# Performance work log

Measured on AMD Instinct MI355X. Metric: run time of the kernel, lower is better.

Reference implementation:

```python
import jax, jax.numpy as jnp
import numpy as np

B, L, N, C, H = 32, 11, 577, 768, 12
HD = C // H  # head dim 64
THRESH = 0.5
NEG = -1e9


def layer_norm(x, g, b, eps=1e-6):
    m = jnp.mean(x, axis=-1, keepdims=True)
    v = jnp.var(x, axis=-1, keepdims=True)
    return (x - m) * jax.lax.rsqrt(v + eps) * g + b


def setup_inputs() -> dict:
    key = jax.random.key(0)
    ks = jax.random.split(key, 8)
    s = 0.02
    return {
        "last_x": jax.random.normal(ks[0], (B, N, C), jnp.float32),
        "attn_scores": jax.random.normal(ks[1], (B, L, N), jnp.float32),
        "norm1_g": jnp.ones((C,), jnp.float32),
        "norm1_b": jnp.zeros((C,), jnp.float32),
        "qkv_w": jax.random.normal(ks[2], (3 * C, C), jnp.float32) * s,
        "qkv_b": jnp.zeros((3 * C,), jnp.float32),
        "proj_w": jax.random.normal(ks[3], (C, C), jnp.float32) * s,
        "proj_b": jnp.zeros((C,), jnp.float32),
        "norm2_g": jnp.ones((C,), jnp.float32),
        "norm2_b": jnp.zeros((C,), jnp.float32),
        "fc1_w": jax.random.normal(ks[4], (4 * C, C), jnp.float32) * s,
        "fc1_b": jnp.zeros((4 * C,), jnp.float32),
        "fc2_w": jax.random.normal(ks[5], (C, 4 * C), jnp.float32) * s,
        "fc2_b": jnp.zeros((C,), jnp.float32),
        "bbn_g": jnp.ones((C,), jnp.float32),
        "bbn_b": jnp.zeros((C,), jnp.float32),
        "out_g": jnp.ones((C,), jnp.float32),
        "out_b": jnp.zeros((C,), jnp.float32),
    }


def prune(attn_scores):
    # scores per block, drop CLS column, softmax over patches, mean over blocks
    ps = jax.nn.softmax(attn_scores[:, :, 1:], axis=-1).mean(axis=1)  # [B, P]
    order = jnp.argsort(ps, axis=1)  # ascending
    sorted_s = jnp.take_along_axis(ps, order, axis=1)
    keep_sorted = jnp.cumsum(sorted_s, axis=1) > THRESH  # drop low-mass prefix
    # scatter back to original patch positions
    pm = jnp.zeros_like(keep_sorted)
    pm = pm.at[jnp.arange(ps.shape[0])[:, None], order].set(keep_sorted)
    # CLS token always kept
    return jnp.concatenate([jnp.ones((ps.shape[0], 1), bool), pm], axis=1)  # [B, N]


def masked_block(x, token_masks, norm1_g, norm1_b, qkv_w, qkv_b, proj_w, proj_b,
                 norm2_g, norm2_b, fc1_w, fc1_b, fc2_w, fc2_b):
    b, n, c = x.shape
    h = layer_norm(x, norm1_g, norm1_b)
    qkv = (h @ qkv_w.T + qkv_b).reshape(b, n, 3, H, HD).transpose(2, 0, 3, 1, 4)
    q, k, v = qkv[0], qkv[1], qkv[2]  # [B, H, N, HD]
    att = jnp.einsum("bhqd,bhkd->bhqk", q, k) * (HD ** -0.5)
    mf = token_masks.astype(x.dtype)
    pair = (mf[:, None, :, None] * mf[:, None, None, :]) > 0  # [B,1,N,N]
    att = jnp.where(pair, att, NEG)
    p = jax.nn.softmax(att, axis=-1)
    p = jnp.where(pair, p, 0.0)  # zero fully-masked rows
    y = jnp.einsum("bhqk,bhkd->bhqd", p, v).transpose(0, 2, 1, 3).reshape(b, n, c)
    y = y @ proj_w.T + proj_b
    x = x + y
    m = layer_norm(x, norm2_g, norm2_b)
    m = jax.nn.gelu(m @ fc1_w.T + fc1_b, approximate=False) @ fc2_w.T + fc2_b
    return x + m


def reference(last_x, attn_scores, norm1_g, norm1_b, qkv_w, qkv_b, proj_w, proj_b,
              norm2_g, norm2_b, fc1_w, fc1_b, fc2_w, fc2_b, bbn_g, bbn_b, out_g, out_b):
    token_masks = prune(attn_scores)  # [B, N] bool
    x = masked_block(last_x, token_masks, norm1_g, norm1_b, qkv_w, qkv_b,
                     proj_w, proj_b, norm2_g, norm2_b, fc1_w, fc1_b, fc2_w, fc2_b)
    x = layer_norm(x, bbn_g, bbn_b)  # backbone final norm
    mf = token_masks.astype(x.dtype)
    pooled = (x * mf[:, :, None]).sum(axis=1) / mf.sum(axis=1, keepdims=True)
    return layer_norm(pooled, out_g, out_b)  # [B, C]
```

## Files before the change

### kernel.cpp

```cpp
#include <hip/hip_runtime.h>

#define B_   32
#define L_   11
#define N_   577
#define C_   768
#define H_   12
#define HD_  64
#define M_   (B_ * N_)
#define NP_  608
#define QT_  32
#define NQT_ 19
#define MCH_ 4616

typedef unsigned int uint32;

typedef short bf16x8 __attribute__((ext_vector_type(8)));
typedef float f32x4  __attribute__((ext_vector_type(4)));

__device__ __forceinline__ unsigned short f2bf(float f) {
    union { float f; uint32 u; } c; c.f = f;
    uint32 u = c.u;
    uint32 r = (u + 0x7FFFu + ((u >> 16) & 1u)) >> 16;
    return (unsigned short)r;
}
__device__ __forceinline__ float bf2f(unsigned short u) {
    union { uint32 u; float f; } c; c.u = ((uint32)u) << 16;
    return c.f;
}
__device__ __forceinline__ float ldval(const float* p, size_t i) { return p[i]; }
__device__ __forceinline__ float ldval(const unsigned short* p, size_t i) { return bf2f(p[i]); }

__device__ __forceinline__ bf16x8 ld_frag(const unsigned short* p) {
    union { uint4 u; bf16x8 v; } c;
    c.u = *reinterpret_cast<const uint4*>(p);
    return c.v;
}

__device__ __forceinline__ void gload_lds16(const unsigned short* g, unsigned short* l) {
    __builtin_amdgcn_global_load_lds(
        (const __attribute__((address_space(1))) unsigned int*)g,
        (__attribute__((address_space(3))) unsigned int*)l, 16, 0, 0);
}

__global__ __launch_bounds__(256) void cast4_kernel(const float* __restrict__ qkvw,
                                                    const float* __restrict__ projw,
                                                    const float* __restrict__ fc1w,
                                                    const float* __restrict__ fc2w,
                                                    unsigned short* __restrict__ dq,
                                                    unsigned short* __restrict__ dp,
                                                    unsigned short* __restrict__ d1,
                                                    unsigned short* __restrict__ d2) {
    int i = blockIdx.x * 256 + threadIdx.x;
    const int N0 = 442368, N1 = 147456, N2 = 589824;
    const float* s; unsigned short* d; int j;
    if (i < N0)                { s = qkvw; d = dq; j = i; }
    else if (i < N0 + N1)      { s = projw; d = dp; j = i - N0; }
    else if (i < N0 + N1 + N2) { s = fc1w;  d = d1; j = i - N0 - N1; }
    else                       { s = fc2w;  d = d2; j = i - N0 - N1 - N2; }
    float4 v = reinterpret_cast<const float4*>(s)[j];
    union { unsigned short us[4]; uint2 u; } o;
    o.us[0] = f2bf(v.x); o.us[1] = f2bf(v.y); o.us[2] = f2bf(v.z); o.us[3] = f2bf(v.w);
    reinterpret_cast<uint2*>(d)[j] = o.u;
}

__global__ __launch_bounds__(256) void prune_kernel(const float* __restrict__ scores,
                                                    float* __restrict__ maskf,
                                                    float* __restrict__ cnt) {
    int b = blockIdx.x, tid = threadIdx.x;
    int lane = tid & 63, wave = tid >> 6;
    __shared__ float ps[576];
    __shared__ float red[4];
    for (int j = tid; j < 576; j += 256) ps[j] = 0.f;
    __syncthreads();
    for (int l = 0; l < L_; ++l) {
        const float* row = scores + ((size_t)b * L_ + l) * N_ + 1;
        float mx = -3.4e38f;
        for (int j = tid; j < 576; j += 256) mx = fmaxf(mx, row[j]);
        for (int off = 32; off; off >>= 1) mx = fmaxf(mx, __shfl_xor(mx, off));
        if (lane == 0) red[wave] = mx;
        __syncthreads();
        mx = fmaxf(fmaxf(red[0], red[1]), fmaxf(red[2], red[3]));
        __syncthreads();
        float s = 0.f;
        for (int j = tid; j < 576; j += 256) s += expf(row[j] - mx);
        for (int off = 32; off; off >>= 1) s += __shfl_xor(s, off);
        if (lane == 0) red[wave] = s;
        __syncthreads();
        s = red[0] + red[1] + red[2] + red[3];
        float inv = 1.f / s;
        for (int j = tid; j < 576; j += 256) ps[j] += expf(row[j] - mx) * inv;
        __syncthreads();
    }
    for (int j = tid; j < 576; j += 256) ps[j] = ps[j] / 11.0f;
    __syncthreads();
    int kept = 0;
    for (int i = tid; i < 576; i += 256) {
        float vi = ps[i];
        float s = 0.f;
        for (int j = 0; j < 576; ++j) {
            float vj = ps[j];
            if (vj < vi || (vj == vi && j <= i)) s += vj;
        }
        int k = (s > 0.5f) ? 1 : 0;
        maskf[b * N_ + 1 + i] = (float)k;
        kept += k;
    }
    __syncthreads();
    for (int off = 32; off; off >>= 1) kept += __shfl_xor(kept, off);
    if (lane == 0) red[wave] = (float)kept;
    __syncthreads();
    if (tid == 0) {
        cnt[b] = red[0] + red[1] + red[2] + red[3] + 1.f;
        maskf[b * N_] = 1.f;
    }
}

template<typename T>
__global__ __launch_bounds__(256) void ln_kernel(const T* __restrict__ x,
                                                 const float* __restrict__ g,
                                                 const float* __restrict__ bta,
                                                 unsigned short* __restrict__ dst_bf,
                                                 float* __restrict__ mu_out,
                                                 float* __restrict__ rs_out) {
    int row = blockIdx.x, tid = threadIdx.x;
    int lane = tid & 63, wave = tid >> 6;
    const T* xr = x + (size_t)row * C_;
    __shared__ float s1[4], s2[4];
    float s = 0.f, sq = 0.f;
    for (int c = tid; c < C_; c += 256) { float v = ldval(xr, c); s += v; sq += v * v; }
    for (int off = 32; off; off >>= 1) { s += __shfl_xor(s, off); sq += __shfl_xor(sq, off); }
    if (lane == 0) { s1[wave] = s; s2[wave] = sq; }
    __syncthreads();
    float ts = s1[0] + s1[1] + s1[2] + s1[3];
    float tq = s2[0] + s2[1] + s2[2] + s2[3];
    float mean = ts / (float)C_;
    float var = tq / (float)C_ - mean * mean;
    float rs = rsqrtf(var + 1e-6f);
    if (mu_out && tid == 0) { mu_out[row] = mean; rs_out[row] = rs; }
    if (dst_bf) {
        for (int c = tid; c < C_; c += 256) {
            float v = (ldval(xr, c) - mean) * rs * g[c] + bta[c];
            dst_bf[(size_t)row * C_ + c] = f2bf(v);
        }
    }
}

template<int MODE, int MI>
__global__ __launch_bounds__(256) void gemm_kernel(const unsigned short* __restrict__ A,
                                                   const unsigned short* __restrict__ Bm,
                                                   const float* __restrict__ bias,
                                                   const float* __restrict__ residf,
                                                   const unsigned short* __restrict__ residb,
                                                   unsigned short* __restrict__ outb,
                                                   unsigned short* __restrict__ qd,
                                                   unsigned short* __restrict__ kd,
                                                   unsigned short* __restrict__ vd,
                                                   int M, int N, int K) {
    constexpr int TILE = MI * 32;
    __shared__ unsigned short As[2][TILE * 32];
    __shared__ unsigned short Bs[2][TILE * 32];
    int bid = blockIdx.x;
    int NT = N / TILE;
    int mt = bid / NT, nt = bid % NT;
    int m0 = mt * TILE, n0 = nt * TILE;
    int tid = threadIdx.x, lane = tid & 63, wave = tid >> 6;
    int ml = lane & 15, quad = lane >> 4;
    int srow = wave * 16 + (lane >> 2);
    int skc = (lane & 3) * 8;
    const unsigned short* ag[MI / 2 == 0 ? 1 : MI / 2];
    const unsigned short* bg[MI / 2 == 0 ? 1 : MI / 2];
#pragma unroll
    for (int jj = 0; jj < MI / 2; ++jj) {
        ag[jj] = A + (size_t)min(m0 + jj * 64 + srow, M - 1) * K + skc;
        bg[jj] = Bm + (size_t)(n0 + jj * 64 + srow) * K + skc;
    }
    int msub = (wave & 1) * (MI * 16), nsub = (wave >> 1) * (MI * 16);
    f32x4 acc[MI][MI] = {};
    for (int k0 = 0; k0 < K; k0 += 64) {
        __syncthreads();
#pragma unroll
        for (int c = 0; c < 2; ++c)
#pragma unroll
        for (int jj = 0; jj < MI / 2; ++jj) {
            gload_lds16(ag[jj] + k0 + c * 32, As[c] + jj * 2048 + wave * 512);
            gload_lds16(bg[jj] + k0 + c * 32, Bs[c] + jj * 2048 + wave * 512);
        }
        asm volatile("s_waitcnt vmcnt(0)" ::: "memory");
        __syncthreads();
#pragma unroll
        for (int c = 0; c < 2; ++c) {
            bf16x8 af[MI], bfm[MI];
#pragma unroll
            for (int i = 0; i < MI; ++i) af[i] = ld_frag(As[c] + (msub + 16 * i + ml) * 32 + quad * 8);
#pragma unroll
            for (int j = 0; j < MI; ++j) bfm[j] = ld_frag(Bs[c] + (nsub + 16 * j + ml) * 32 + quad * 8);
#pragma unroll
            for (int i = 0; i < MI; ++i)
#pragma unroll
                for (int j = 0; j < MI; ++j)
                    acc[i][j] = __builtin_amdgcn_mfma_f32_16x16x32_bf16(af[i], bfm[j], acc[i][j], 0, 0, 0);
        }
    }
#pragma unroll
    for (int i = 0; i < MI; ++i)
#pragma unroll
    for (int j = 0; j < MI; ++j)
#pragma unroll
    for (int r = 0; r < 4; ++r) {
        int row = m0 + msub + 16 * i + quad * 4 + r;
        if (row >= M) continue;
        int col = n0 + nsub + 16 * j + ml;
        float v = acc[i][j][r] + bias[col];
        if (MODE == 0) {
            int b = row / N_, t = row - b * N_;
            int f = col;
            if (f < 768) {
                qd[((size_t)(b * H_ + (f >> 6)) * N_ + t) * HD_ + (f & 63)] = f2bf(v * 0.125f);
            } else if (f < 1536) {
                f -= 768;
                kd[((size_t)(b * H_ + (f >> 6)) * N_ + t) * HD_ + (f & 63)] = f2bf(v);
            } else {
                f -= 1536;
                vd[((size_t)(b * H_ + (f >> 6)) * HD_ + (f & 63)) * NP_ + t] = f2bf(v);
            }
        } else if (MODE == 1) {
            outb[(size_t)row * N + col] = f2bf(v + residf[(size_t)row * N + col]);
        } else if (MODE == 2) {
            float gl = 0.5f * v * (1.f + erff(v * 0.70710678118654752f));
            outb[(size_t)row * N + col] = f2bf(gl);
        } else {
            outb[(size_t)row * N + col] = f2bf(v + bf2f(residb[(size_t)row * N + col]));
        }
    }
}

__global__ __launch_bounds__(256, 4) void attn_kernel(const unsigned short* __restrict__ qb,
                                                      const unsigned short* __restrict__ kb,
                                                      const unsigned short* __restrict__ vt,
                                                      const float* __restrict__ maskf,
                                                      unsigned short* __restrict__ ybf) {
    int bid = blockIdx.x;
    int xcd = bid & 7, g = bid >> 3;
    int bh = (g / NQT_) * 8 + xcd;
    int qt = g % NQT_;
    int h = bh % H_, b = bh / H_;
    int q0 = qt * QT_;
    int tid = threadIdx.x, lane = tid & 63, wave = tid >> 6;
    int ml = lane & 15, quad = lane >> 4, kq = quad * 8;
    __shared__ __align__(16) unsigned short P[QT_][616];
    __shared__ float wred[4][QT_];

    const float* bmask = maskf + (size_t)b * N_;
    float mrowv[2][4];
#pragma unroll
    for (int s = 0; s < 2; ++s)
#pragma unroll
    for (int r = 0; r < 4; ++r) {
        int t = q0 + s * 16 + quad * 4 + r;
        mrowv[s][r] = (t < N_) ? bmask[t] : 0.f;
    }
    const unsigned short* qbase = qb + (size_t)(b * H_ + h) * N_ * HD_;
    const unsigned short* kbase = kb + (size_t)(b * H_ + h) * N_ * HD_;
    bf16x8 aq[2][2];
#pragma unroll
    for (int s = 0; s < 2; ++s) {
        int qrow = min(q0 + s * 16 + ml, N_ - 1);
        aq[s][0] = ld_frag(qbase + (size_t)qrow * HD_ + kq);
        aq[s][1] = ld_frag(qbase + (size_t)qrow * HD_ + kq + 32);
    }
    float ls[2][4] = {};
#pragma unroll
    for (int t = 0; t < 10; ++t) {
        int nt = wave + 4 * t;
        if (nt < NP_ / 16) {
            int col = nt * 16 + ml;
            int krow = min(col, N_ - 1);
            bf16x8 bk0 = ld_frag(kbase + (size_t)krow * HD_ + kq);
            bf16x8 bk1 = ld_frag(kbase + (size_t)krow * HD_ + kq + 32);
            bool keep = (col < N_) && (bmask[col] > 0.f);
#pragma unroll
            for (int s = 0; s < 2; ++s) {
                f32x4 a = {0.f, 0.f, 0.f, 0.f};
                a = __builtin_amdgcn_mfma_f32_16x16x32_bf16(aq[s][0], bk0, a, 0, 0, 0);
                a = __builtin_amdgcn_mfma_f32_16x16x32_bf16(aq[s][1], bk1, a, 0, 0, 0);
#pragma unroll
                for (int r = 0; r < 4; ++r) {
                    float e = keep ? __expf(a[r]) : 0.f;
                    ls[s][r] += e;
                    P[s * 16 + quad * 4 + r][col] = f2bf(e);
                }
            }
        }
    }
#pragma unroll
    for (int s = 0; s < 2; ++s)
#pragma unroll
    for (int r = 0; r < 4; ++r) {
#pragma unroll
        for (int off = 1; off < 16; off <<= 1) ls[s][r] += __shfl_xor(ls[s][r], off);
    }
    if (ml == 0) {
#pragma unroll
        for (int s = 0; s < 2; ++s)
#pragma unroll
        for (int r = 0; r < 4; ++r) wred[wave][s * 16 + quad * 4 + r] = ls[s][r];
    }
    __syncthreads();
    float inv[2][4];
#pragma unroll
    for (int s = 0; s < 2; ++s)
#pragma unroll
    for (int r = 0; r < 4; ++r) {
        int row = s * 16 + quad * 4 + r;
        float sum = wred[0][row] + wred[1][row] + wred[2][row] + wred[3][row];
        inv[s][r] = mrowv[s][r] / sum;
    }
    const unsigned short* vrow = vt + ((size_t)(b * H_ + h) * HD_ + wave * 16 + ml) * NP_ + kq;
    f32x4 acc[2] = {};
#pragma unroll
    for (int t = 0; t < 19; ++t) {
        bf16x8 vb = ld_frag(vrow + t * 32);
#pragma unroll
        for (int s = 0; s < 2; ++s) {
            bf16x8 pa = ld_frag(&P[s * 16 + ml][kq + t * 32]);
            acc[s] = __builtin_amdgcn_mfma_f32_16x16x32_bf16(pa, vb, acc[s], 0, 0, 0);
        }
    }
#pragma unroll
    for (int s = 0; s < 2; ++s)
#pragma unroll
    for (int r = 0; r < 4; ++r) {
        int t = q0 + s * 16 + quad * 4 + r;
        if (t < N_)
            ybf[((size_t)(b * N_ + t)) * C_ + h * HD_ + wave * 16 + ml] = f2bf(acc[s][r] * inv[s][r]);
    }
}

__global__ __launch_bounds__(256) void pool_kernel(const unsigned short* __restrict__ x2,
                                                   const float* __restrict__ mu,
                                                   const float* __restrict__ rs,
                                                   const float* __restrict__ maskf,
                                                   float* __restrict__ praw) {
    int c = blockIdx.x * 256 + threadIdx.x;
    int tchunk = blockIdx.y;
    int b = blockIdx.z;
    int t0 = tchunk * 73, t1 = min(t0 + 73, N_);
    float s = 0.f;
    for (int t = t0; t < t1; ++t) {
        int row = b * N_ + t;
        float m = maskf[row];
        if (m > 0.f) s += (bf2f(x2[(size_t)row * C_ + c]) - mu[row]) * rs[row];
    }
    atomicAdd(&praw[b * C_ + c], s);
}

__global__ __launch_bounds__(256) void final_kernel(const float* __restrict__ praw,
                                                    const float* __restrict__ cnt,
                                                    const float* __restrict__ bg,
                                                    const float* __restrict__ bb,
                                                    const float* __restrict__ og,
                                                    const float* __restrict__ ob,
                                                    float* __restrict__ out) {
    int b = blockIdx.x, tid = threadIdx.x;
    int lane = tid & 63, wave = tid >> 6;
    __shared__ float u[C_];
    __shared__ float r1[4], r2[4];
    float inv = 1.f / cnt[b];
    float s = 0.f, sq = 0.f;
    for (int c = tid; c < C_; c += 256) {
        float v = bg[c] * praw[b * C_ + c] * inv + bb[c];
        u[c] = v; s += v; sq += v * v;
    }
    for (int off = 32; off; off >>= 1) { s += __shfl_xor(s, off); sq += __shfl_xor(sq, off); }
    if (lane == 0) { r1[wave] = s; r2[wave] = sq; }
    __syncthreads();
    float ts = r1[0] + r1[1] + r1[2] + r1[3];
    float tq = r2[0] + r2[1] + r2[2] + r2[3];
    float mean = ts / (float)C_;
    float var = tq / (float)C_ - mean * mean;
    float rstd = rsqrtf(var + 1e-6f);
    for (int c = tid; c < C_; c += 256)
        out[b * C_ + c] = (u[c] - mean) * rstd * og[c] + ob[c];
}

extern "C" void kernel_launch(void* const* d_in, const int* in_sizes, int n_in,
                              void* d_out, int out_size, void* d_ws, size_t ws_size,
                              hipStream_t stream) {
    const float* last_x  = (const float*)d_in[0];
    const float* scores  = (const float*)d_in[1];
    const float* n1g     = (const float*)d_in[2];
    const float* n1b     = (const float*)d_in[3];
    const float* qkv_w   = (const float*)d_in[4];
    const float* qkv_b   = (const float*)d_in[5];
    const float* proj_w  = (const float*)d_in[6];
    const float* proj_b  = (const float*)d_in[7];
    const float* n2g     = (const float*)d_in[8];
    const float* n2b     = (const float*)d_in[9];
    const float* fc1_w   = (const float*)d_in[10];
    const float* fc1_b   = (const float*)d_in[11];
    const float* fc2_w   = (const float*)d_in[12];
    const float* fc2_b   = (const float*)d_in[13];
    const float* bbn_g   = (const float*)d_in[14];
    const float* bbn_b   = (const float*)d_in[15];
    const float* out_g   = (const float*)d_in[16];
    const float* out_b   = (const float*)d_in[17];
    float* out = (float*)d_out;

    char* w = (char*)d_ws;
    size_t off = 0;
    auto alloc = [&](size_t bytes) -> char* {
        off = (off + 255) & ~(size_t)255;
        char* p = w + off;
        off += bytes;
        return p;
    };
    unsigned short* wq = (unsigned short*)alloc((size_t)2304 * 768 * 2);
    unsigned short* wp = (unsigned short*)alloc((size_t)768 * 768 * 2);
    unsigned short* w1 = (unsigned short*)alloc((size_t)3072 * 768 * 2);
    unsigned short* w2 = (unsigned short*)alloc((size_t)768 * 3072 * 2);
    float* maskf = (float*)alloc((size_t)M_ * 4);
    float* cnt   = (float*)alloc(32 * 4);
    float* mu    = (float*)alloc((size_t)M_ * 4);
    float* rs    = (float*)alloc((size_t)M_ * 4);
    float* praw  = (float*)alloc((size_t)B_ * C_ * 4);
    unsigned short* h_bf = (unsigned short*)alloc((size_t)M_ * C_ * 2);
    unsigned short* q_bf = (unsigned short*)alloc((size_t)B_ * H_ * N_ * HD_ * 2);
    unsigned short* k_bf = (unsigned short*)alloc((size_t)B_ * H_ * N_ * HD_ * 2);
    unsigned short* vt   = (unsigned short*)alloc((size_t)B_ * H_ * HD_ * NP_ * 2);
    unsigned short* y_bf = h_bf;
    unsigned short* m_bf = q_bf;
    unsigned short* x1   = vt;
    unsigned short* x2   = k_bf;

    size_t act_need = (size_t)M_ * 3072 * 2;
    bool big = (((off + 255) & ~(size_t)255) + act_need) <= ws_size;
    unsigned short* act = big ? (unsigned short*)alloc(act_need) : h_bf;

    cast4_kernel<<<6912, 256, 0, stream>>>(qkv_w, proj_w, fc1_w, fc2_w, wq, wp, w1, w2);
    prune_kernel<<<B_, 256, 0, stream>>>(scores, maskf, cnt);
    ln_kernel<float><<<M_, 256, 0, stream>>>(last_x, n1g, n1b, h_bf, nullptr, nullptr);
    gemm_kernel<0, 4><<<((M_ + 127) / 128) * (2304 / 128), 256, 0, stream>>>(
        h_bf, wq, qkv_b, nullptr, nullptr, nullptr, q_bf, k_bf, vt, M_, 2304, C_);
    attn_kernel<<<B_ * H_ * NQT_, 256, 0, stream>>>(q_bf, k_bf, vt, maskf, y_bf);
    gemm_kernel<1, 4><<<((M_ + 127) / 128) * (768 / 128), 256, 0, stream>>>(
        y_bf, wp, proj_b, last_x, nullptr, x1, nullptr, nullptr, nullptr, M_, C_, C_);
    ln_kernel<unsigned short><<<M_, 256, 0, stream>>>(x1, n2g, n2b, m_bf, nullptr, nullptr);
    if (big) {
        gemm_kernel<2, 4><<<((M_ + 127) / 128) * (3072 / 128), 256, 0, stream>>>(
            m_bf, w1, fc1_b, nullptr, nullptr, act, nullptr, nullptr, nullptr, M_, 3072, C_);
        gemm_kernel<3, 4><<<((M_ + 127) / 128) * (768 / 128), 256, 0, stream>>>(
            act, w2, fc2_b, nullptr, x1, x2, nullptr, nullptr, nullptr, M_, C_, 3072);
    } else {
        for (int c = 0; c < 4; ++c) {
            int r0 = c * MCH_;
            gemm_kernel<2, 4><<<((MCH_ + 127) / 128) * (3072 / 128), 256, 0, stream>>>(
                m_bf + (size_t)r0 * C_, w1, fc1_b, nullptr, nullptr, act,
                nullptr, nullptr, nullptr, MCH_, 3072, C_);
            gemm_kernel<3, 4><<<((MCH_ + 127) / 128) * (768 / 128), 256, 0, stream>>>(
                act, w2, fc2_b, nullptr, x1 + (size_t)r0 * C_, x2 + (size_t)r0 * C_,
                nullptr, nullptr, nullptr, MCH_, 768, 3072);
        }
    }
    ln_kernel<unsigned short><<<M_, 256, 0, stream>>>(x2, bbn_g, bbn_b, nullptr, mu, rs);
    hipMemsetAsync(praw, 0, (size_t)B_ * C_ * 4, stream);
    dim3 pg(3, 8, B_);
    pool_kernel<<<pg, 256, 0, stream>>>(x2, mu, rs, maskf, praw);
    final_kernel<<<B_, 256, 0, stream>>>(praw, cnt, bbn_g, bbn_b, out_g, out_b, out);
    (void)in_sizes; (void)n_in; (void)out_size;
}
```

Baseline: 1.169 ms.

## Group GEMM tiles by N-chunk and relayout LDS staging to avoid bank conflicts

Block indices are remapped so that consecutive workgroups walk down M inside a chunk of CH column tiles. This is meant to keep a small set of weight tiles hot in L2 across concurrently running blocks. The global-to-LDS staging mapping is also changed so each wave stores rows in a k-quad-major layout. Fragment reads then become contiguous 16-byte accesses per lane group, which is meant to cut LDS bank conflicts. The risk is that the new layout must match the direct-to-LDS load ordering exactly, and a different raster could reduce A-operand reuse.

```diff
diff --git a/kernel.cpp b/kernel.cpp
--- a/kernel.cpp
+++ b/kernel.cpp
@@ -155,18 +155,23 @@
                                                    unsigned short* __restrict__ qd,
                                                    unsigned short* __restrict__ kd,
                                                    unsigned short* __restrict__ vd,
-                                                   int M, int N, int K) {
+                                                   int M, int N, int K, int CH) {
     constexpr int TILE = MI * 32;
     __shared__ unsigned short As[2][TILE * 32];
     __shared__ unsigned short Bs[2][TILE * 32];
     int bid = blockIdx.x;
     int NT = N / TILE;
-    int mt = bid / NT, nt = bid % NT;
+    int MT = gridDim.x / NT;
+    int per = MT * CH;
+    int chunk = bid / per;
+    int rloc = bid - chunk * per;
+    int mt = rloc / CH;
+    int nt = chunk * CH + (rloc - mt * CH);
     int m0 = mt * TILE, n0 = nt * TILE;
     int tid = threadIdx.x, lane = tid & 63, wave = tid >> 6;
     int ml = lane & 15, quad = lane >> 4;
-    int srow = wave * 16 + (lane >> 2);
-    int skc = (lane & 3) * 8;
+    int srow = wave * 16 + (lane & 15);
+    int skc = (lane >> 4) * 8;
     const unsigned short* ag[MI / 2 == 0 ? 1 : MI / 2];
     const unsigned short* bg[MI / 2 == 0 ? 1 : MI / 2];
 #pragma unroll
@@ -175,6 +180,7 @@
         bg[jj] = Bm + (size_t)(n0 + jj * 64 + srow) * K + skc;
     }
     int msub = (wave & 1) * (MI * 16), nsub = (wave >> 1) * (MI * 16);
+    int mg0 = msub >> 4, ng0 = nsub >> 4;
     f32x4 acc[MI][MI] = {};
     for (int k0 = 0; k0 < K; k0 += 64) {
         __syncthreads();
@@ -191,9 +197,9 @@
         for (int c = 0; c < 2; ++c) {
             bf16x8 af[MI], bfm[MI];
 #pragma unroll
-            for (int i = 0; i < MI; ++i) af[i] = ld_frag(As[c] + (msub + 16 * i + ml) * 32 + quad * 8);
-#pragma unroll
-            for (int j = 0; j < MI; ++j) bfm[j] = ld_frag(Bs[c] + (nsub + 16 * j + ml) * 32 + quad * 8);
+            for (int i = 0; i < MI; ++i) af[i] = ld_frag(As[c] + (mg0 + i) * 512 + quad * 128 + ml * 8);
+#pragma unroll
+            for (int j = 0; j < MI; ++j) bfm[j] = ld_frag(Bs[c] + (ng0 + j) * 512 + quad * 128 + ml * 8);
 #pragma unroll
             for (int i = 0; i < MI; ++i)
 #pragma unroll
@@ -440,25 +446,25 @@
     prune_kernel<<<B_, 256, 0, stream>>>(scores, maskf, cnt);
     ln_kernel<float><<<M_, 256, 0, stream>>>(last_x, n1g, n1b, h_bf, nullptr, nullptr);
     gemm_kernel<0, 4><<<((M_ + 127) / 128) * (2304 / 128), 256, 0, stream>>>(
-        h_bf, wq, qkv_b, nullptr, nullptr, nullptr, q_bf, k_bf, vt, M_, 2304, C_);
+        h_bf, wq, qkv_b, nullptr, nullptr, nullptr, q_bf, k_bf, vt, M_, 2304, C_, 6);
     attn_kernel<<<B_ * H_ * NQT_, 256, 0, stream>>>(q_bf, k_bf, vt, maskf, y_bf);
     gemm_kernel<1, 4><<<((M_ + 127) / 128) * (768 / 128), 256, 0, stream>>>(
-        y_bf, wp, proj_b, last_x, nullptr, x1, nullptr, nullptr, nullptr, M_, C_, C_);
+        y_bf, wp, proj_b, last_x, nullptr, x1, nullptr, nullptr, nullptr, M_, C_, C_, 6);
     ln_kernel<unsigned short><<<M_, 256, 0, stream>>>(x1, n2g, n2b, m_bf, nullptr, nullptr);
     if (big) {
         gemm_kernel<2, 4><<<((M_ + 127) / 128) * (3072 / 128), 256, 0, stream>>>(
-            m_bf, w1, fc1_b, nullptr, nullptr, act, nullptr, nullptr, nullptr, M_, 3072, C_);
+            m_bf, w1, fc1_b, nullptr, nullptr, act, nullptr, nullptr, nullptr, M_, 3072, C_, 8);
         gemm_kernel<3, 4><<<((M_ + 127) / 128) * (768 / 128), 256, 0, stream>>>(
-            act, w2, fc2_b, nullptr, x1, x2, nullptr, nullptr, nullptr, M_, C_, 3072);
+            act, w2, fc2_b, nullptr, x1, x2, nullptr, nullptr, nullptr, M_, C_, 3072, 2);
     } else {
         for (int c = 0; c < 4; ++c) {
             int r0 = c * MCH_;
             gemm_kernel<2, 4><<<((MCH_ + 127) / 128) * (3072 / 128), 256, 0, stream>>>(
                 m_bf + (size_t)r0 * C_, w1, fc1_b, nullptr, nullptr, act,
-                nullptr, nullptr, nullptr, MCH_, 3072, C_);
+                nullptr, nullptr, nullptr, MCH_, 3072, C_, 8);
             gemm_kernel<3, 4><<<((MCH_ + 127) / 128) * (768 / 128), 256, 0, stream>>>(
                 act, w2, fc2_b, nullptr, x1 + (size_t)r0 * C_, x2 + (size_t)r0 * C_,
-                nullptr, nullptr, nullptr, MCH_, 768, 3072);
+                nullptr, nullptr, nullptr, MCH_, 768, 3072, 2);
         }
     }
     ln_kernel<unsigned short><<<M_, 256, 0, stream>>>(x2, bbn_g, bbn_b, nullptr, mu, rs);
```

Result: slower. 1.337 ms (+14.3%).
